# Optimization experiments

Hardware: AMD Instinct MI355X
Metric: run time of the kernel (lower is better)

The kernel has to match this reference:

```python
import jax, jax.numpy as jnp
import numpy as np
from functools import partial

# Static problem sizes (equal-sized, sorted batch assumed; batch = repeat(arange(B), NPTS))
B, NPTS, C_IN = 8, 4096, 64
M = 1024      # centroids per cloud = ratio(0.25) * NPTS
K = 64        # max_num_neighbors in radius()
R = 0.2       # ball-query radius
EPS = 1e-5    # BatchNorm eps


def fps_single(pos, m):
    """Farthest point sampling on one cloud. pos: [n,3]. Deterministic start at index 0."""
    n = pos.shape[0]
    def step(carry, _):
        dists, last = carry
        d = jnp.sum(jnp.square(pos - pos[last]), axis=-1)
        dists = jnp.minimum(dists, d)
        nxt = jnp.argmax(dists)
        return (dists, nxt), nxt
    init = (jnp.full((n,), 1e10, pos.dtype), jnp.int32(0))
    _, rest = jax.lax.scan(step, init, None, length=m - 1)
    return jnp.concatenate([jnp.zeros((1,), rest.dtype), rest])  # [m]


def bn_relu(h, W, g, b, mask):
    """Linear(no bias) + BatchNorm1d (training-mode batch stats over valid edges) + ReLU.
    h: [B,M,K,Cin], mask: [B,M,K] (1 = real neighbor edge)."""
    h = h @ W
    mk = mask[..., None]
    cnt = jnp.maximum(jnp.sum(mask), 1.0)
    mu = jnp.sum(h * mk, axis=(0, 1, 2)) / cnt
    var = jnp.sum(jnp.square(h - mu) * mk, axis=(0, 1, 2)) / cnt
    return jax.nn.relu((h - mu) * jax.lax.rsqrt(var + EPS) * g + b)


def forward(x, pos, batch, W1, g1, b1, W2, g2, b2, W3, g3, b3):
    posb = pos.reshape(B, NPTS, 3)
    xb = x.reshape(B, NPTS, C_IN)
    # --- FPS (indices are non-differentiable constants) ---
    idx = jax.lax.stop_gradient(jax.vmap(partial(fps_single, m=M))(posb))   # [B,M]
    cent = jnp.take_along_axis(posb, idx[..., None], axis=1)                # [B,M,3]
    # --- radius ball query, capped at K nearest within R (deterministic) ---
    d2 = jnp.sum(jnp.square(jax.lax.stop_gradient(cent)[:, :, None]
                            - jax.lax.stop_gradient(posb)[:, None]), axis=-1)  # [B,M,n]
    vals, nbr = jax.lax.top_k(jnp.where(d2 <= R * R, -d2, -jnp.inf), K)        # [B,M,K]
    mask = (vals > -jnp.inf).astype(pos.dtype)   # centroid itself (d2=0) always valid
    # --- gather neighbors, local MLP on [x_j, pos_j - pos_i], max-aggregate ---
    gather = jax.vmap(lambda a, i: a[i])
    pj = gather(posb, nbr)                                     # [B,M,K,3]
    xj = gather(xb, nbr)                                       # [B,M,K,C]
    h = jnp.concatenate([xj, pj - cent[:, :, None]], axis=-1)  # [B,M,K,C+3]
    h = bn_relu(h, W1, g1, b1, mask)
    h = bn_relu(h, W2, g2, b2, mask)
    h = bn_relu(h, W3, g3, b3, mask)
    x_out = jnp.max(jnp.where(mask[..., None] > 0, h, -jnp.inf), axis=2)  # [B,M,128]
    bsel = jnp.repeat(jnp.arange(B, dtype=batch.dtype), M)
    return x_out.reshape(B * M, -1), cent.reshape(B * M, 3), bsel


def setup_inputs():
    key = jax.random.key(0)
    ks = jax.random.split(key, 11)
    N = B * NPTS
    x = jax.random.normal(ks[0], (N, C_IN), jnp.float32)
    pos = jax.random.uniform(ks[1], (N, 3), jnp.float32)   # unit cube point clouds
    batch = jnp.repeat(jnp.arange(B, dtype=jnp.int32), NPTS)
    ch = [C_IN + 3, 64, 64, 128]
    def lin(k, i, o):
        return jax.random.normal(k, (i, o), jnp.float32) * (1.0 / np.sqrt(i))
    W1, W2, W3 = lin(ks[2], ch[0], ch[1]), lin(ks[3], ch[1], ch[2]), lin(ks[4], ch[2], ch[3])
    g1 = 1.0 + 0.1 * jax.random.normal(ks[5], (ch[1],), jnp.float32)
    g2 = 1.0 + 0.1 * jax.random.normal(ks[6], (ch[2],), jnp.float32)
    g3 = 1.0 + 0.1 * jax.random.normal(ks[7], (ch[3],), jnp.float32)
    b1 = 0.05 * jax.random.normal(ks[8], (ch[1],), jnp.float32)
    b2 = 0.05 * jax.random.normal(ks[9], (ch[2],), jnp.float32)
    b3 = 0.05 * jax.random.normal(ks[10], (ch[3],), jnp.float32)
    return {"x": x, "pos": pos, "batch": batch,
            "W1": W1, "g1": g1, "b1": b1,
            "W2": W2, "g2": g2, "b2": b2,
            "W3": W3, "g3": g3, "b3": b3}


def reference(x, pos, batch, W1, g1, b1, W2, g2, b2, W3, g3, b3):
    return forward(x, pos, batch, W1, g1, b1, W2, g2, b2, W3, g3, b3)
```

## Files before the change

kernel.cpp:

```cpp
#include <hip/hip_runtime.h>
#include <stdint.h>

#define NB   8
#define NPTS 4096
#define CINV 64
#define MC   1024
#define KNB  64
#define NE   (NB*MC*KNB)
#define K1   67
#define CH1  64
#define CH2  64
#define CH3  128
#define NSLOT 64
#define CAP  2048
#define NTASK (NB*MC)
#define NBLK 256

typedef unsigned short u16;
typedef unsigned int   u32;
typedef unsigned long long u64;

static __device__ __forceinline__ float bf2f(u16 b){ return __uint_as_float(((u32)b)<<16); }
static __device__ __forceinline__ u16  f2bf(float f){
  u32 u = __float_as_uint(f);
  return (u16)((u + 0x7fffu + ((u>>16)&1u)) >> 16);
}
static __device__ __forceinline__ float d2ref(float ax,float ay,float az,
                                              float bx,float by,float bz){
  float dx = ax-bx, dy = ay-by, dz = az-bz;
  return __fadd_rn(__fadd_rn(__fmul_rn(dx,dx), __fmul_rn(dy,dy)), __fmul_rn(dz,dz));
}
template<int CTRL, int RMASK>
static __device__ __forceinline__ float dppmaxstep(float v){
  int t = __builtin_amdgcn_update_dpp(__float_as_int(v), __float_as_int(v),
                                      CTRL, RMASK, 0xF, false);
  return fmaxf(v, __int_as_float(t));
}
template<int CTRL, int RMASK>
static __device__ __forceinline__ float dppminstep(float v){
  int t = __builtin_amdgcn_update_dpp(__float_as_int(v), __float_as_int(v),
                                      CTRL, RMASK, 0xF, false);
  return fminf(v, __int_as_float(t));
}
template<int CTRL, int RMASK>
static __device__ __forceinline__ float dppaddstep(float v){
  int t = __builtin_amdgcn_update_dpp(0, __float_as_int(v), CTRL, RMASK, 0xF, false);
  return v + __int_as_float(t);
}
static __device__ __forceinline__ float dppsum16(float v){
  v = dppaddstep<0xB1,0xF>(v); v = dppaddstep<0x4E,0xF>(v);
  v = dppaddstep<0x141,0xF>(v); v = dppaddstep<0x140,0xF>(v);
  return v;
}
static __device__ __forceinline__ float dppmax16(float v){
  v = dppmaxstep<0xB1,0xF>(v); v = dppmaxstep<0x4E,0xF>(v);
  v = dppmaxstep<0x141,0xF>(v); v = dppmaxstep<0x140,0xF>(v);
  return v;
}
static __device__ __forceinline__ float dppmin16(float v){
  v = dppminstep<0xB1,0xF>(v); v = dppminstep<0x4E,0xF>(v);
  v = dppminstep<0x141,0xF>(v); v = dppminstep<0x140,0xF>(v);
  return v;
}
static __device__ __forceinline__ double kpack(float d, int ni){
  return __hiloint2double(__float_as_int(d), ni);
}
template<int CTRL, int RMASK>
static __device__ __forceinline__ double dppk64(double k){
  int hi = __double2hiint(k), lo = __double2loint(k);
  int thi = __builtin_amdgcn_update_dpp(hi, hi, CTRL, RMASK, 0xF, false);
  int tlo = __builtin_amdgcn_update_dpp(lo, lo, CTRL, RMASK, 0xF, false);
  return fmax(k, __hiloint2double(thi, tlo));
}

struct FpsL {
  float px[NPTS], py[NPTS], pz[NPTS];
  int   sIdx[MC];
  double candD[8];
  float4 cbuf[16];
};
struct WkL {
  u64   keys[CAP];
  float Hs[64*69];
  int   nbrS[64];
  float red[8][16][4];
  float cxyz[3];
  int   scnt;
  int   task;
};
union FrontL { FpsL f; WkL w; };

__global__ __launch_bounds__(512) void k_front(const float* __restrict__ x,
                                               const float* __restrict__ pos,
                                               float* __restrict__ centf,
                                               float* __restrict__ out_cent,
                                               float* __restrict__ out_bsel,
                                               const float* __restrict__ W1,
                                               float* __restrict__ Spart,
                                               u16* __restrict__ y1g,
                                               int* __restrict__ cntpc,
                                               int* __restrict__ cnt_total,
                                               int* __restrict__ progress,
                                               int* __restrict__ taskctr) {
  __shared__ FrontL L;
  const int tid = threadIdx.x;

  if (blockIdx.x < NB) {
    const int b = blockIdx.x;
    for (int i = tid; i < NPTS; i += 512) {
      size_t o = ((size_t)b*NPTS + i)*3;
      L.f.px[i] = pos[o]; L.f.py[i] = pos[o+1]; L.f.pz[i] = pos[o+2];
    }
    __syncthreads();
    if (tid >= 256) return;

    float cxr[16], cyr[16], czr[16], dist[16];
    int nio[16];
    #pragma unroll
    for (int j = 0; j < 16; ++j) {
      int p = tid*16 + j;
      cxr[j] = L.f.px[p]; cyr[j] = L.f.py[p]; czr[j] = L.f.pz[p];
      dist[j] = 1e10f;
      nio[j] = ~p;
    }
    const int lane = tid & 63, w = tid >> 6;
    float qx = L.f.px[0], qy = L.f.py[0], qz = L.f.pz[0];
    if (tid == 0) {
      L.f.sIdx[0] = 0;
      L.f.cbuf[0] = make_float4(qx, qy, qz, 0.f);
    }

    for (int it = 1; it < MC; ++it) {
      #pragma unroll
      for (int j = 0; j < 16; ++j) {
        float d = d2ref(cxr[j], cyr[j], czr[j], qx, qy, qz);
        dist[j] = fminf(dist[j], d);
      }
      double t0 = fmax(kpack(dist[0],  nio[0]),  kpack(dist[1],  nio[1]));
      double t1 = fmax(kpack(dist[2],  nio[2]),  kpack(dist[3],  nio[3]));
      double t2 = fmax(kpack(dist[4],  nio[4]),  kpack(dist[5],  nio[5]));
      double t3 = fmax(kpack(dist[6],  nio[6]),  kpack(dist[7],  nio[7]));
      double t4 = fmax(kpack(dist[8],  nio[8]),  kpack(dist[9],  nio[9]));
      double t5 = fmax(kpack(dist[10], nio[10]), kpack(dist[11], nio[11]));
      double t6 = fmax(kpack(dist[12], nio[12]), kpack(dist[13], nio[13]));
      double t7 = fmax(kpack(dist[14], nio[14]), kpack(dist[15], nio[15]));
      double u0 = fmax(t0, t1), u1 = fmax(t2, t3), u2 = fmax(t4, t5), u3 = fmax(t6, t7);
      double bk = fmax(fmax(u0, u1), fmax(u2, u3));
      bk = dppk64<0xB1,0xF>(bk);
      bk = dppk64<0x4E,0xF>(bk);
      bk = dppk64<0x141,0xF>(bk);
      bk = dppk64<0x140,0xF>(bk);
      bk = dppk64<0x142,0xA>(bk);
      bk = dppk64<0x143,0xC>(bk);
      if (lane == 63) L.f.candD[(it & 1)*4 + w] = bk;
      __syncthreads();
      double ck = L.f.candD[(it & 1)*4 + (lane & 3)];
      ck = dppk64<0xB1,0xF>(ck);
      ck = dppk64<0x4E,0xF>(ck);
      int wi = (int)(~(u32)__double2loint(ck));
      qx = L.f.px[wi]; qy = L.f.py[wi]; qz = L.f.pz[wi];
      if ((it & 15) == 0 && tid < 16) {
        int mrow = it - 16 + tid;
        float4 cc = L.f.cbuf[tid];
        int r = b*MC + mrow;
        centf[r*3+0] = cc.x; centf[r*3+1] = cc.y; centf[r*3+2] = cc.z;
        if (tid == 0)
          __hip_atomic_store(progress + b, it, __ATOMIC_RELEASE, __HIP_MEMORY_SCOPE_AGENT);
      }
      if (tid == 0) {
        L.f.sIdx[it] = wi;
        L.f.cbuf[it & 15] = make_float4(qx, qy, qz, 0.f);
      }
    }
    __syncthreads();
    if (tid < 16) {
      int mrow = MC - 16 + tid;
      float4 cc = L.f.cbuf[tid];
      int r = b*MC + mrow;
      centf[r*3+0] = cc.x; centf[r*3+1] = cc.y; centf[r*3+2] = cc.z;
      if (tid == 0)
        __hip_atomic_store(progress + b, MC, __ATOMIC_RELEASE, __HIP_MEMORY_SCOPE_AGENT);
    }
    for (int m2_ = tid; m2_ < MC; m2_ += 256) {
      int i = L.f.sIdx[m2_];
      int r = b*MC + m2_;
      out_cent[r*3+0] = L.f.px[i]; out_cent[r*3+1] = L.f.py[i]; out_cent[r*3+2] = L.f.pz[i];
      out_bsel[r] = (float)b;
    }
    return;
  }

  for (;;) {
    if (tid == 0) {
      int t = atomicAdd(taskctr, 1);
      L.w.task = t;
      if (t < NTASK) {
        int m = t >> 3, b = t & 7;
        while (__hip_atomic_load(progress + b, __ATOMIC_ACQUIRE, __HIP_MEMORY_SCOPE_AGENT) < m + 1)
          __builtin_amdgcn_s_sleep(8);
        int bm = b*MC + m;
        L.w.cxyz[0] = __hip_atomic_load(centf + bm*3 + 0, __ATOMIC_RELAXED, __HIP_MEMORY_SCOPE_AGENT);
        L.w.cxyz[1] = __hip_atomic_load(centf + bm*3 + 1, __ATOMIC_RELAXED, __HIP_MEMORY_SCOPE_AGENT);
        L.w.cxyz[2] = __hip_atomic_load(centf + bm*3 + 2, __ATOMIC_RELAXED, __HIP_MEMORY_SCOPE_AGENT);
      }
      L.w.scnt = 0;
    }
    __syncthreads();
    const int t = L.w.task;
    if (t >= NTASK) return;
    const int m = t >> 3, b = t & 7, bm = b*MC + m;
    const float cx = L.w.cxyz[0], cy = L.w.cxyz[1], cz = L.w.cxyz[2];

    for (int i = tid; i < NPTS; i += 512) {
      size_t o = ((size_t)b*NPTS + i)*3;
      float d = d2ref(cx, cy, cz, pos[o], pos[o+1], pos[o+2]);
      if (d <= 0.04f) {
        int p = atomicAdd(&L.w.scnt, 1);
        if (p < CAP) L.w.keys[p] = ((u64)__float_as_uint(d) << 32) | (u32)i;
      }
    }
    __syncthreads();
    int n = L.w.scnt; if (n > CAP) n = CAP;
    int P = 64; while (P < n) P <<= 1;
    for (int i = n + tid; i < P; i += 512) L.w.keys[i] = ~0ull;
    __syncthreads();
    for (int ks = 2; ks <= P; ks <<= 1)
      for (int js = ks >> 1; js > 0; js >>= 1) {
        for (int i = tid; i < P; i += 512) {
          int l = i ^ js;
          if (l > i) {
            u64 a = L.w.keys[i], c = L.w.keys[l];
            bool up = ((i & ks) == 0);
            if ((a > c) == up) { L.w.keys[i] = c; L.w.keys[l] = a; }
          }
        }
        __syncthreads();
      }
    const int c = n < KNB ? n : KNB;
    if (tid < KNB) L.w.nbrS[tid] = (tid < c) ? (int)(u32)(L.w.keys[tid] & 0xffffffffu) : 0;
    if (tid == 0) { cntpc[bm] = c; atomicAdd(cnt_total, c); }
    __syncthreads();

    {
      const int ge = tid >> 3, qb = tid & 7;
      const float4* xr = (const float4*)(x + ((size_t)(b*NPTS + L.w.nbrS[ge]))*CINV);
      #pragma unroll
      for (int rep = 0; rep < 2; ++rep) {
        int q = qb + rep*8;
        float4 v = xr[q];
        float* d = L.w.Hs + ge*69 + q*4;
        d[0] = v.x; d[1] = v.y; d[2] = v.z; d[3] = v.w;
      }
    }
    if (tid < 64) {
      int row = b*NPTS + L.w.nbrS[tid];
      L.w.Hs[tid*69+64] = pos[(size_t)row*3+0] - cx;
      L.w.Hs[tid*69+65] = pos[(size_t)row*3+1] - cy;
      L.w.Hs[tid*69+66] = pos[(size_t)row*3+2] - cz;
    }
    __syncthreads();

    const int edge = tid & 63;
    const int col  = __builtin_amdgcn_readfirstlane(tid >> 6);
    float acc[8];
    #pragma unroll
    for (int j = 0; j < 8; ++j) acc[j] = 0.f;
    const float* hrow = L.w.Hs + edge*69;
    const float* wcol = W1 + col*8;
    for (int k = 0; k < K1; ++k) {
      float hk = hrow[k];
      const float4* w4 = (const float4*)(wcol + k*CH1);
      float4 a = w4[0], bq = w4[1];
      acc[0] = fmaf(hk, a.x,  acc[0]); acc[1] = fmaf(hk, a.y,  acc[1]);
      acc[2] = fmaf(hk, a.z,  acc[2]); acc[3] = fmaf(hk, a.w,  acc[3]);
      acc[4] = fmaf(hk, bq.x, acc[4]); acc[5] = fmaf(hk, bq.y, acc[5]);
      acc[6] = fmaf(hk, bq.z, acc[6]); acc[7] = fmaf(hk, bq.w, acc[7]);
    }
    const bool valid = edge < c;
    #pragma unroll
    for (int j = 0; j < 8; ++j) acc[j] = valid ? acc[j] : 0.f;
    u32* dst = (u32*)(y1g + ((size_t)bm*64 + edge)*CH1 + col*8);
    #pragma unroll
    for (int j = 0; j < 4; ++j)
      dst[j] = (u32)f2bf(acc[2*j]) | ((u32)f2bf(acc[2*j+1]) << 16);
    #pragma unroll
    for (int j = 0; j < 8; ++j) {
      float s = dppsum16(acc[j]);
      float q = dppsum16(acc[j]*acc[j]);
      if ((edge & 15) == 0) {
        L.w.red[col][j][edge>>4]   = s;
        L.w.red[col][8+j][edge>>4] = q;
      }
    }
    __syncthreads();
    const int slot = bm & (NSLOT-1);
    if (tid < 64) {
      float4 g = *(const float4*)&L.w.red[tid>>3][tid&7][0];
      atomicAdd(&Spart[slot*256 + tid], (g.x+g.y)+(g.z+g.w));
    } else if (tid < 128) {
      int cc = tid - 64;
      float4 g = *(const float4*)&L.w.red[cc>>3][8+(cc&7)][0];
      atomicAdd(&Spart[slot*256 + 128 + cc], (g.x+g.y)+(g.z+g.w));
    }
  }
}

__global__ __launch_bounds__(256) void k_s2(const u16* __restrict__ y1g,
                                            const float* __restrict__ SC,
                                            const float* __restrict__ W2,
                                            const int* __restrict__ cntpc,
                                            float* __restrict__ Spart,
                                            u16* __restrict__ y2g) {
  __shared__ float Hs[64*65];
  __shared__ float ABs[128];
  __shared__ float red[4][32][4];
  __shared__ int   cntS;
  const int tid = threadIdx.x, bm = blockIdx.x;
  if (tid == 0) cntS = cntpc[bm];
  if (tid < 128) ABs[tid] = SC[tid];
  __syncthreads();
  {
    const u32* yt = (const u32*)y1g + (size_t)bm*2048;
    #pragma unroll
    for (int rep = 0; rep < 8; ++rep) {
      int g = rep*256 + tid;
      int e = g >> 5, c2 = g & 31, ch = c2*2;
      u32 v = yt[g];
      float lo = fmaxf(fmaf(bf2f((u16)(v & 0xffff)), ABs[ch],   ABs[64+ch]),   0.f);
      float hi = fmaxf(fmaf(bf2f((u16)(v >> 16)),    ABs[ch+1], ABs[64+ch+1]), 0.f);
      Hs[e*65 + ch] = lo; Hs[e*65 + ch + 1] = hi;
    }
  }
  __syncthreads();

  const int edge = tid & 63;
  const int col  = __builtin_amdgcn_readfirstlane(tid >> 6);
  float acc[16];
  #pragma unroll
  for (int j = 0; j < 16; ++j) acc[j] = 0.f;
  const float* hrow = Hs + edge*65;
  const float* wcol = W2 + col*16;
  for (int k = 0; k < CH1; ++k) {
    float hk = hrow[k];
    const float4* w4 = (const float4*)(wcol + k*CH2);
    #pragma unroll
    for (int q = 0; q < 4; ++q) {
      float4 wv = w4[q];
      acc[q*4+0] = fmaf(hk, wv.x, acc[q*4+0]);
      acc[q*4+1] = fmaf(hk, wv.y, acc[q*4+1]);
      acc[q*4+2] = fmaf(hk, wv.z, acc[q*4+2]);
      acc[q*4+3] = fmaf(hk, wv.w, acc[q*4+3]);
    }
  }
  const bool valid = edge < cntS;
  #pragma unroll
  for (int j = 0; j < 16; ++j) acc[j] = valid ? acc[j] : 0.f;
  u32* dst = (u32*)(y2g + ((size_t)bm*64 + edge)*CH2 + col*16);
  #pragma unroll
  for (int j = 0; j < 8; ++j)
    dst[j] = (u32)f2bf(acc[2*j]) | ((u32)f2bf(acc[2*j+1]) << 16);
  #pragma unroll
  for (int j = 0; j < 16; ++j) {
    float s = dppsum16(acc[j]);
    float q = dppsum16(acc[j]*acc[j]);
    if ((edge & 15) == 0) {
      red[col][j][edge>>4]    = s;
      red[col][16+j][edge>>4] = q;
    }
  }
  __syncthreads();
  const int slot = bm & (NSLOT-1);
  if (tid < 64) {
    float4 g = *(const float4*)&red[tid>>4][tid&15][0];
    atomicAdd(&Spart[slot*256 + tid], (g.x+g.y)+(g.z+g.w));
  } else if (tid < 128) {
    int c = tid - 64;
    float4 g = *(const float4*)&red[c>>4][16+(c&15)][0];
    atomicAdd(&Spart[slot*256 + 128 + c], (g.x+g.y)+(g.z+g.w));
  }
}

__global__ __launch_bounds__(256) void k_s3(const u16* __restrict__ y2g,
                                            const float* __restrict__ SC,
                                            const float* __restrict__ W3,
                                            const int* __restrict__ cntpc,
                                            float* __restrict__ Spart,
                                            float* __restrict__ mxmn) {
  __shared__ float Hs[64*65];
  __shared__ float ABs[128];
  __shared__ float red[4][64][4];
  __shared__ float redm[4][64][4];
  __shared__ int   cntS;
  const int tid = threadIdx.x, bm = blockIdx.x;
  if (tid == 0) cntS = cntpc[bm];
  if (tid < 128) ABs[tid] = SC[128 + tid];
  __syncthreads();
  {
    const u32* yt = (const u32*)y2g + (size_t)bm*2048;
    #pragma unroll
    for (int rep = 0; rep < 8; ++rep) {
      int g = rep*256 + tid;
      int e = g >> 5, c2 = g & 31, ch = c2*2;
      u32 v = yt[g];
      float lo = fmaxf(fmaf(bf2f((u16)(v & 0xffff)), ABs[ch],   ABs[64+ch]),   0.f);
      float hi = fmaxf(fmaf(bf2f((u16)(v >> 16)),    ABs[ch+1], ABs[64+ch+1]), 0.f);
      Hs[e*65 + ch] = lo; Hs[e*65 + ch + 1] = hi;
    }
  }
  __syncthreads();

  const int edge = tid & 63;
  const int col  = __builtin_amdgcn_readfirstlane(tid >> 6);
  float acc[32];
  #pragma unroll
  for (int j = 0; j < 32; ++j) acc[j] = 0.f;
  const float* hrow = Hs + edge*65;
  const float* wcol = W3 + col*32;
  for (int k = 0; k < CH2; ++k) {
    float hk = hrow[k];
    const float4* w4 = (const float4*)(wcol + k*CH3);
    #pragma unroll
    for (int q = 0; q < 8; ++q) {
      float4 wv = w4[q];
      acc[q*4+0] = fmaf(hk, wv.x, acc[q*4+0]);
      acc[q*4+1] = fmaf(hk, wv.y, acc[q*4+1]);
      acc[q*4+2] = fmaf(hk, wv.z, acc[q*4+2]);
      acc[q*4+3] = fmaf(hk, wv.w, acc[q*4+3]);
    }
  }
  const bool valid = edge < cntS;
  #pragma unroll
  for (int j = 0; j < 32; ++j) {
    float mxv = valid ? acc[j] : -1e30f;
    float mnv = valid ? acc[j] :  1e30f;
    float av  = valid ? acc[j] : 0.f;
    float s  = dppsum16(av);
    float q  = dppsum16(av*av);
    float mx = dppmax16(mxv);
    float mn = dppmin16(mnv);
    if ((edge & 15) == 0) {
      red[col][j][edge>>4]     = s;
      red[col][32+j][edge>>4]  = q;
      redm[col][j][edge>>4]    = mx;
      redm[col][32+j][edge>>4] = mn;
    }
  }
  __syncthreads();
  const int slot = bm & (NSLOT-1);
  if (tid < 128) {
    float4 g = *(const float4*)&red[tid>>5][tid&31][0];
    atomicAdd(&Spart[slot*256 + tid], (g.x+g.y)+(g.z+g.w));
    float4 gm = *(const float4*)&redm[tid>>5][tid&31][0];
    mxmn[(size_t)bm*256 + tid] = fmaxf(fmaxf(gm.x, gm.y), fmaxf(gm.z, gm.w));
  } else {
    int c = tid - 128;
    float4 g = *(const float4*)&red[c>>5][32+(c&31)][0];
    atomicAdd(&Spart[slot*256 + 128 + c], (g.x+g.y)+(g.z+g.w));
    float4 gm = *(const float4*)&redm[c>>5][32+(c&31)][0];
    mxmn[(size_t)bm*256 + 128 + c] = fminf(fminf(gm.x, gm.y), fminf(gm.z, gm.w));
  }
}

__global__ __launch_bounds__(128) void k_s4(const float* __restrict__ mxmn,
                                            const float* __restrict__ SC,
                                            float* __restrict__ out0) {
  const int tid = threadIdx.x, bm = blockIdx.x;
  const float a = SC[256 + tid], b = SC[384 + tid];
  const float mx = mxmn[(size_t)bm*256 + tid];
  const float mn = mxmn[(size_t)bm*256 + 128 + tid];
  const float v = (a > 0.f) ? mx : mn;
  out0[(size_t)bm*CH3 + tid] = fmaxf(fmaf(v, a, b), 0.f);
}

__global__ void k_finalize(const float* __restrict__ Spart,
                           const float* __restrict__ g, const float* __restrict__ bb,
                           const int* __restrict__ cnt_total,
                           float* __restrict__ Aout, float* __restrict__ Bout, int C) {
  int c = threadIdx.x;
  if (c < C) {
    float s = 0.f, q = 0.f;
    for (int sl = 0; sl < NSLOT; ++sl) {
      s += Spart[sl*256 + c];
      q += Spart[sl*256 + 128 + c];
    }
    float n = (float)(*cnt_total); if (n < 1.f) n = 1.f;
    float mu  = s / n;
    float var = q / n - mu*mu; if (var < 0.f) var = 0.f;
    float inv = 1.0f / sqrtf(var + 1e-5f);
    float a = g[c] * inv;
    Aout[c] = a;
    Bout[c] = bb[c] - mu*a;
  }
}

extern "C" void kernel_launch(void* const* d_in, const int* in_sizes, int n_in,
                              void* d_out, int out_size, void* d_ws, size_t ws_size,
                              hipStream_t stream) {
  (void)in_sizes; (void)n_in; (void)out_size; (void)ws_size;
  const float* x   = (const float*)d_in[0];
  const float* pos = (const float*)d_in[1];
  const float* W1  = (const float*)d_in[3];
  const float* g1  = (const float*)d_in[4];
  const float* b1  = (const float*)d_in[5];
  const float* W2  = (const float*)d_in[6];
  const float* g2  = (const float*)d_in[7];
  const float* b2  = (const float*)d_in[8];
  const float* W3  = (const float*)d_in[9];
  const float* g3  = (const float*)d_in[10];
  const float* b3  = (const float*)d_in[11];

  float* out0     = (float*)d_out;
  float* out_cent = out0 + (size_t)NB*MC*CH3;
  float* out_bsel = out_cent + (size_t)NB*MC*3;

  char* base = (char*)d_ws;
  size_t off = 0;
  auto carve = [&](size_t bytes) -> char* {
    char* p = base + off;
    off = (off + bytes + 255) & ~(size_t)255;
    return p;
  };
  float* centf = (float*)carve(sizeof(float)*NB*MC*3);
  int*   cntpc = (int*)  carve(sizeof(int)*NB*MC);
  char*  zeroblk = carve(256 + 3*NSLOT*256*sizeof(float));
  int*   cnt_total = (int*)zeroblk;
  int*   taskctr   = cnt_total + 1;
  int*   progress  = cnt_total + 2;
  float* Sp1 = (float*)(zeroblk + 256);
  float* Sp2 = Sp1 + NSLOT*256;
  float* Sp3 = Sp2 + NSLOT*256;
  float* SC = (float*)carve(512*sizeof(float));
  u16* y1g = (u16*)carve((size_t)NE*CH1*2);
  u16* y2g = (u16*)carve((size_t)NE*CH2*2);
  float* mxmn = (float*)carve((size_t)NB*MC*256*sizeof(float));

  hipMemsetAsync(zeroblk, 0, 256 + 3*NSLOT*256*sizeof(float), stream);
  k_front<<<NBLK, 512, 0, stream>>>(x, pos, centf, out_cent, out_bsel,
                                    W1, Sp1, y1g, cntpc, cnt_total, progress, taskctr);
  k_finalize<<<1, 128, 0, stream>>>(Sp1, g1, b1, cnt_total, SC + 0,   SC + 64,  CH1);
  dim3 sg(NB*MC), sb(256);
  k_s2<<<sg, sb, 0, stream>>>(y1g, SC, W2, cntpc, Sp2, y2g);
  k_finalize<<<1, 128, 0, stream>>>(Sp2, g2, b2, cnt_total, SC + 128, SC + 192, CH2);
  k_s3<<<sg, sb, 0, stream>>>(y2g, SC, W3, cntpc, Sp3, mxmn);
  k_finalize<<<1, 128, 0, stream>>>(Sp3, g3, b3, cnt_total, SC + 256, SC + 384, CH3);
  k_s4<<<sg, 128, 0, stream>>>(mxmn, SC, out0);
}
```

Measured before the change: 1.040 ms.

## Compute layer-3 GEMM in k_s3 with bf16 MFMA instead of scalar FMA

```diff
diff --git a/kernel.cpp b/kernel.cpp
--- a/kernel.cpp
+++ b/kernel.cpp
@@ -20,6 +20,9 @@
 typedef unsigned int   u32;
 typedef unsigned long long u64;
 
+using f32x4  = __attribute__((ext_vector_type(4))) float;
+using bf16x8 = __attribute__((ext_vector_type(8))) short;
+
 static __device__ __forceinline__ float bf2f(u16 b){ return __uint_as_float(((u32)b)<<16); }
 static __device__ __forceinline__ u16  f2bf(float f){
   u32 u = __float_as_uint(f);
@@ -50,16 +53,6 @@
 static __device__ __forceinline__ float dppsum16(float v){
   v = dppaddstep<0xB1,0xF>(v); v = dppaddstep<0x4E,0xF>(v);
   v = dppaddstep<0x141,0xF>(v); v = dppaddstep<0x140,0xF>(v);
-  return v;
-}
-static __device__ __forceinline__ float dppmax16(float v){
-  v = dppmaxstep<0xB1,0xF>(v); v = dppmaxstep<0x4E,0xF>(v);
-  v = dppmaxstep<0x141,0xF>(v); v = dppmaxstep<0x140,0xF>(v);
-  return v;
-}
-static __device__ __forceinline__ float dppmin16(float v){
-  v = dppminstep<0xB1,0xF>(v); v = dppminstep<0x4E,0xF>(v);
-  v = dppminstep<0x141,0xF>(v); v = dppminstep<0x140,0xF>(v);
   return v;
 }
 static __device__ __forceinline__ double kpack(float d, int ni){
@@ -380,16 +373,26 @@
   }
 }
 
+__global__ void k_wconv(const float* __restrict__ W3, u16* __restrict__ W3f) {
+  int t = blockIdx.x*256 + threadIdx.x;
+  int T = t >> 9, lane = (t >> 3) & 63, j = t & 7;
+  int n = (T >> 1)*16 + (lane & 15);
+  int k = (T & 1)*32 + (lane >> 4)*8 + j;
+  W3f[t] = f2bf(W3[k*CH3 + n]);
+}
+
 __global__ __launch_bounds__(256) void k_s3(const u16* __restrict__ y2g,
                                             const float* __restrict__ SC,
-                                            const float* __restrict__ W3,
+                                            const u16* __restrict__ W3f,
                                             const int* __restrict__ cntpc,
                                             float* __restrict__ Spart,
                                             float* __restrict__ mxmn) {
-  __shared__ float Hs[64*65];
+  __shared__ u16   Hb[64*72];
   __shared__ float ABs[128];
-  __shared__ float red[4][64][4];
-  __shared__ float redm[4][64][4];
+  __shared__ float redS[4][32][4];
+  __shared__ float redQ[4][32][4];
+  __shared__ float redM[4][32][4];
+  __shared__ float redN[4][32][4];
   __shared__ int   cntS;
   const int tid = threadIdx.x, bm = blockIdx.x;
   if (tid == 0) cntS = cntpc[bm];
@@ -400,63 +403,79 @@
     #pragma unroll
     for (int rep = 0; rep < 8; ++rep) {
       int g = rep*256 + tid;
-      int e = g >> 5, c2 = g & 31, ch = c2*2;
+      int e = g >> 5, ch = (g & 31)*2;
       u32 v = yt[g];
       float lo = fmaxf(fmaf(bf2f((u16)(v & 0xffff)), ABs[ch],   ABs[64+ch]),   0.f);
       float hi = fmaxf(fmaf(bf2f((u16)(v >> 16)),    ABs[ch+1], ABs[64+ch+1]), 0.f);
-      Hs[e*65 + ch] = lo; Hs[e*65 + ch + 1] = hi;
+      *(u32*)&Hb[e*72 + ch] = (u32)f2bf(lo) | ((u32)f2bf(hi) << 16);
     }
   }
   __syncthreads();
 
-  const int edge = tid & 63;
-  const int col  = __builtin_amdgcn_readfirstlane(tid >> 6);
-  float acc[32];
-  #pragma unroll
-  for (int j = 0; j < 32; ++j) acc[j] = 0.f;
-  const float* hrow = Hs + edge*65;
-  const float* wcol = W3 + col*32;
-  for (int k = 0; k < CH2; ++k) {
-    float hk = hrow[k];
-    const float4* w4 = (const float4*)(wcol + k*CH3);
-    #pragma unroll
-    for (int q = 0; q < 8; ++q) {
-      float4 wv = w4[q];
-      acc[q*4+0] = fmaf(hk, wv.x, acc[q*4+0]);
-      acc[q*4+1] = fmaf(hk, wv.y, acc[q*4+1]);
-      acc[q*4+2] = fmaf(hk, wv.z, acc[q*4+2]);
-      acc[q*4+3] = fmaf(hk, wv.w, acc[q*4+3]);
-    }
-  }
-  const bool valid = edge < cntS;
-  #pragma unroll
-  for (int j = 0; j < 32; ++j) {
-    float mxv = valid ? acc[j] : -1e30f;
-    float mnv = valid ? acc[j] :  1e30f;
-    float av  = valid ? acc[j] : 0.f;
-    float s  = dppsum16(av);
-    float q  = dppsum16(av*av);
-    float mx = dppmax16(mxv);
-    float mn = dppmin16(mnv);
-    if ((edge & 15) == 0) {
-      red[col][j][edge>>4]     = s;
-      red[col][32+j][edge>>4]  = q;
-      redm[col][j][edge>>4]    = mx;
-      redm[col][32+j][edge>>4] = mn;
-    }
+  const int lane = tid & 63;
+  const int wv   = __builtin_amdgcn_readfirstlane(tid >> 6);
+  const int r16  = lane & 15, g4 = lane >> 4;
+  const int cnt  = cntS;
+
+  bf16x8 bfr[2][2];
+  #pragma unroll
+  for (int Nt = 0; Nt < 2; ++Nt)
+    #pragma unroll
+    for (int Kt = 0; Kt < 2; ++Kt)
+      bfr[Nt][Kt] = *(const bf16x8*)&W3f[(((wv*2 + Nt)*2 + Kt)*64 + lane)*8];
+
+  f32x4 acc[4][2];
+  #pragma unroll
+  for (int Mt = 0; Mt < 4; ++Mt)
+    #pragma unroll
+    for (int Nt = 0; Nt < 2; ++Nt)
+      acc[Mt][Nt] = (f32x4){0.f, 0.f, 0.f, 0.f};
+
+  #pragma unroll
+  for (int Kt = 0; Kt < 2; ++Kt) {
+    #pragma unroll
+    for (int Mt = 0; Mt < 4; ++Mt) {
+      bf16x8 afr = *(const bf16x8*)&Hb[(Mt*16 + r16)*72 + Kt*32 + g4*8];
+      #pragma unroll
+      for (int Nt = 0; Nt < 2; ++Nt)
+        acc[Mt][Nt] = __builtin_amdgcn_mfma_f32_16x16x32_bf16(afr, bfr[Nt][Kt],
+                                                              acc[Mt][Nt], 0, 0, 0);
+    }
+  }
+
+  #pragma unroll
+  for (int Nt = 0; Nt < 2; ++Nt) {
+    float s = 0.f, q = 0.f, mx = -1e30f, mn = 1e30f;
+    #pragma unroll
+    for (int Mt = 0; Mt < 4; ++Mt) {
+      #pragma unroll
+      for (int rr = 0; rr < 4; ++rr) {
+        int row = Mt*16 + g4*4 + rr;
+        float v = acc[Mt][Nt][rr];
+        bool valid = row < cnt;
+        float av = valid ? v : 0.f;
+        s += av; q = fmaf(av, av, q);
+        mx = fmaxf(mx, valid ? v : -1e30f);
+        mn = fminf(mn, valid ? v :  1e30f);
+      }
+    }
+    redS[wv][Nt*16 + r16][g4] = s;
+    redQ[wv][Nt*16 + r16][g4] = q;
+    redM[wv][Nt*16 + r16][g4] = mx;
+    redN[wv][Nt*16 + r16][g4] = mn;
   }
   __syncthreads();
   const int slot = bm & (NSLOT-1);
   if (tid < 128) {
-    float4 g = *(const float4*)&red[tid>>5][tid&31][0];
+    float4 g = *(const float4*)&redS[tid>>5][tid&31][0];
     atomicAdd(&Spart[slot*256 + tid], (g.x+g.y)+(g.z+g.w));
-    float4 gm = *(const float4*)&redm[tid>>5][tid&31][0];
+    float4 gm = *(const float4*)&redM[tid>>5][tid&31][0];
     mxmn[(size_t)bm*256 + tid] = fmaxf(fmaxf(gm.x, gm.y), fmaxf(gm.z, gm.w));
   } else {
     int c = tid - 128;
-    float4 g = *(const float4*)&red[c>>5][32+(c&31)][0];
+    float4 g = *(const float4*)&redQ[c>>5][c&31][0];
     atomicAdd(&Spart[slot*256 + 128 + c], (g.x+g.y)+(g.z+g.w));
-    float4 gm = *(const float4*)&redm[c>>5][32+(c&31)][0];
+    float4 gm = *(const float4*)&redN[c>>5][c&31][0];
     mxmn[(size_t)bm*256 + 128 + c] = fminf(fminf(gm.x, gm.y), fminf(gm.z, gm.w));
   }
 }
@@ -533,15 +552,17 @@
   u16* y1g = (u16*)carve((size_t)NE*CH1*2);
   u16* y2g = (u16*)carve((size_t)NE*CH2*2);
   float* mxmn = (float*)carve((size_t)NB*MC*256*sizeof(float));
+  u16* W3f = (u16*)carve(16*64*8*sizeof(u16));
 
   hipMemsetAsync(zeroblk, 0, 256 + 3*NSLOT*256*sizeof(float), stream);
+  k_wconv<<<32, 256, 0, stream>>>(W3, W3f);
   k_front<<<NBLK, 512, 0, stream>>>(x, pos, centf, out_cent, out_bsel,
                                     W1, Sp1, y1g, cntpc, cnt_total, progress, taskctr);
   k_finalize<<<1, 128, 0, stream>>>(Sp1, g1, b1, cnt_total, SC + 0,   SC + 64,  CH1);
   dim3 sg(NB*MC), sb(256);
   k_s2<<<sg, sb, 0, stream>>>(y1g, SC, W2, cntpc, Sp2, y2g);
   k_finalize<<<1, 128, 0, stream>>>(Sp2, g2, b2, cnt_total, SC + 128, SC + 192, CH2);
-  k_s3<<<sg, sb, 0, stream>>>(y2g, SC, W3, cntpc, Sp3, mxmn);
+  k_s3<<<sg, sb, 0, stream>>>(y2g, SC, W3f, cntpc, Sp3, mxmn);
   k_finalize<<<1, 128, 0, stream>>>(Sp3, g3, b3, cnt_total, SC + 256, SC + 384, CH3);
   k_s4<<<sg, 128, 0, stream>>>(mxmn, SC, out0);
 }
```

New measurement: 900.0 us. -13.4%, faster.
